# Optimization experiments

Measured on AMD Instinct MI355X. Metric: run time of the kernel, lower is better.

The kernel has to match this reference:

```python
import jax, jax.numpy as jnp
import numpy as np

H = 768
NH = 12
HD = H // NH


def setup_inputs() -> dict:
    key = jax.random.key(0)
    ks = jax.random.split(key, 12)
    B, S = 2, 2048
    s = 1.0 / np.sqrt(H)
    inp = {
        "hidden_states": jax.random.normal(ks[0], (B, S, H), dtype=jnp.float32),
        "attention_mask": jnp.ones((B, S), dtype=jnp.float32),
        "Wq": jax.random.normal(ks[1], (H, H), dtype=jnp.float32) * s,
        "bq": jnp.zeros((H,), dtype=jnp.float32),
        "Wk": jax.random.normal(ks[2], (H, H), dtype=jnp.float32) * s,
        "bk": jnp.zeros((H,), dtype=jnp.float32),
        "Wv": jax.random.normal(ks[3], (H, H), dtype=jnp.float32) * s,
        "bv": jnp.zeros((H,), dtype=jnp.float32),
        "Wo": jax.random.normal(ks[4], (H, H), dtype=jnp.float32) * s,
        "bo": jnp.zeros((H,), dtype=jnp.float32),
        "ln_gamma": jnp.ones((H,), dtype=jnp.float32),
        "ln_beta": jnp.zeros((H,), dtype=jnp.float32),
    }
    return inp


def _split_heads(x):
    # [B,S,H] -> [B,NH,S,HD]
    B, S, _ = x.shape
    return x.reshape(B, S, NH, HD).transpose(0, 2, 1, 3)


def reference(hidden_states, attention_mask, Wq, bq, Wk, bk, Wv, bv, Wo, bo, ln_gamma, ln_beta):
    x = hidden_states
    q = _split_heads(x @ Wq.T + bq)
    k = _split_heads(x @ Wk.T + bk)
    v = _split_heads(x @ Wv.T + bv)
    # scores: [B,NH,S,S]
    scores = jnp.einsum("bhqd,bhkd->bhqk", q, k) / jnp.sqrt(jnp.float32(HD))
    mask = (1.0 - attention_mask)[:, None, None, :] * -10000.0
    scores = scores + mask
    probs = jax.nn.softmax(scores, axis=-1)  # dropout is identity at inference
    ctx = jnp.einsum("bhqk,bhkd->bhqd", probs, v)
    B, _, S, _ = ctx.shape
    ctx = ctx.transpose(0, 2, 1, 3).reshape(B, S, H)
    out = ctx @ Wo.T + bo
    y = out + x
    mu = jnp.mean(y, axis=-1, keepdims=True)
    var = jnp.var(y, axis=-1, keepdims=True)
    y = (y - mu) / jnp.sqrt(var + 1e-5)
    return y * ln_gamma + ln_beta
```

## Files before the change

kernel.cpp:

```cpp
#include <hip/hip_runtime.h>
#include <math.h>

#define HH 768
#define NHEADS 12
#define HDIM 64
#define SEQ 2048
#define NB 2
#define L2E 1.44269504088896f

typedef __attribute__((ext_vector_type(8))) short s8v;
typedef __attribute__((ext_vector_type(4))) short s4v;
typedef __attribute__((ext_vector_type(4))) float f4v;

static __device__ inline short f2bf(float f) {
    union { float f; unsigned u; } v; v.f = f;
    unsigned r = v.u + 0x7fff + ((v.u >> 16) & 1);
    return (short)(r >> 16);
}

#if __has_builtin(__builtin_amdgcn_exp2f)
#define EXP2(x) __builtin_amdgcn_exp2f(x)
#else
#define EXP2(x) __expf((x) * 0.6931471805599453f)
#endif

__device__ __forceinline__ unsigned cvt_pk_bf16(float a, float b) {
    unsigned r;
    asm("v_cvt_pk_bf16_f32 %0, %1, %2" : "=v"(r) : "v"(a), "v"(b));
    return r;
}

__device__ __forceinline__ void gld16(const void* g, void* l) {
    __builtin_amdgcn_global_load_lds(
        (const __attribute__((address_space(1))) void*)g,
        (__attribute__((address_space(3))) void*)l, 16, 0, 0);
}

#define XV8   393216
#define WV8   73728
__global__ __launch_bounds__(256)
void cvt_kernel(const float* __restrict__ X, short* __restrict__ Xb,
                const float* __restrict__ W0, short* __restrict__ W0b,
                const float* __restrict__ W1, short* __restrict__ W1b,
                const float* __restrict__ W2, short* __restrict__ W2b,
                const float* __restrict__ W3, short* __restrict__ W3b)
{
    int gid = blockIdx.x * 256 + threadIdx.x;
    const float* src; short* dst; size_t off;
    if      (gid < XV8)            { src = X;  dst = Xb;  off = gid; }
    else if (gid < XV8 + WV8)      { src = W0; dst = W0b; off = gid - XV8; }
    else if (gid < XV8 + 2*WV8)    { src = W1; dst = W1b; off = gid - XV8 - WV8; }
    else if (gid < XV8 + 3*WV8)    { src = W2; dst = W2b; off = gid - XV8 - 2*WV8; }
    else if (gid < XV8 + 4*WV8)    { src = W3; dst = W3b; off = gid - XV8 - 3*WV8; }
    else return;
    off *= 8;
    float4 a = *(const float4*)(src + off);
    float4 b = *(const float4*)(src + off + 4);
    s8v o;
    o[0] = f2bf(a.x); o[1] = f2bf(a.y); o[2] = f2bf(a.z); o[3] = f2bf(a.w);
    o[4] = f2bf(b.x); o[5] = f2bf(b.y); o[6] = f2bf(b.z); o[7] = f2bf(b.w);
    *(s8v*)(dst + off) = o;
}

template<int EPI>
__global__ __launch_bounds__(256)
void gemm_mfma(const short* __restrict__ A,
               const short* __restrict__ Wq, const short* __restrict__ Wk,
               const short* __restrict__ Wv,
               const float* __restrict__ bq, const float* __restrict__ bk,
               const float* __restrict__ bv,
               short* __restrict__ Qo, short* __restrict__ Ko, short* __restrict__ Vo,
               const float* __restrict__ Xres, float* __restrict__ Fo)
{
    __shared__ __align__(16) short As[128*32];
    __shared__ __align__(16) short Bs[128*32];

    const int tid  = threadIdx.x;
    const int w    = tid >> 6;
    const int lane = tid & 63;
    const int g    = lane >> 4;
    const int r    = lane & 15;
    const int wr   = w >> 1;
    const int wc   = w & 1;
    const int m0   = blockIdx.y * 128;

    int n0;
    const short* Wb; const float* bias; short* outp; float scale;
    if (EPI == 0) {
        const int seg = blockIdx.x / 6;
        n0 = (blockIdx.x % 6) * 128;
        Wb   = seg == 0 ? Wq : seg == 1 ? Wk : Wv;
        bias = seg == 0 ? bq : seg == 1 ? bk : bv;
        outp = seg == 0 ? Qo : seg == 1 ? Ko : Vo;
        scale = seg == 0 ? (0.125f * L2E) : 1.0f;
    } else {
        n0 = blockIdx.x * 128;
        Wb = Wq; bias = bq; outp = nullptr; scale = 1.0f;
    }

    const int lrow = lane >> 2;
    const int lcol = (lane & 3) * 8;
    const short* Ag0 = A  + (size_t)(m0 + w*32 + lrow) * HH + lcol;
    const short* Bg0 = Wb + (size_t)(n0 + w*32 + lrow) * HH + lcol;
    short* Al0 = As + (w*32)      * 32;
    short* Al1 = As + (w*32 + 16) * 32;
    short* Bl0 = Bs + (w*32)      * 32;
    short* Bl1 = Bs + (w*32 + 16) * 32;

    f4v acc[4][4];
    #pragma unroll
    for (int i = 0; i < 4; i++)
        #pragma unroll
        for (int j = 0; j < 4; j++) acc[i][j] = (f4v){0.f,0.f,0.f,0.f};

    for (int kt = 0; kt < HH/32; ++kt) {
        const int k0 = kt * 32;
        gld16(Ag0 + k0,           Al0);
        gld16(Ag0 + k0 + 16*HH,   Al1);
        gld16(Bg0 + k0,           Bl0);
        gld16(Bg0 + k0 + 16*HH,   Bl1);
        __syncthreads();

        s8v af[4], bf[4];
        #pragma unroll
        for (int mi = 0; mi < 4; mi++)
            af[mi] = *(const s8v*)(As + (wr*64 + mi*16 + r)*32 + g*8);
        #pragma unroll
        for (int ni = 0; ni < 4; ni++)
            bf[ni] = *(const s8v*)(Bs + (wc*64 + ni*16 + r)*32 + g*8);
        __builtin_amdgcn_s_setprio(1);
        #pragma unroll
        for (int mi = 0; mi < 4; mi++)
            #pragma unroll
            for (int ni = 0; ni < 4; ni++)
                acc[mi][ni] = __builtin_amdgcn_mfma_f32_16x16x32_bf16(af[mi], bf[ni], acc[mi][ni], 0, 0, 0);
        __builtin_amdgcn_s_setprio(0);
        __syncthreads();
    }

    if (EPI == 0) {
        #pragma unroll
        for (int mi = 0; mi < 4; mi++) {
            #pragma unroll
            for (int j = 0; j < 4; j++) {
                const int m = m0 + wr*64 + mi*16 + 4*g + j;
                const int bb = m >> 11;
                const int s  = m & 2047;
                #pragma unroll
                for (int ni = 0; ni < 4; ni++) {
                    const int n = n0 + wc*64 + ni*16 + r;
                    const int h = n >> 6;
                    const int d = n & 63;
                    outp[((size_t)((bb*NHEADS + h)*SEQ) + s)*HDIM + d] =
                        f2bf((acc[mi][ni][j] + bias[n]) * scale);
                }
            }
        }
    } else {
        #pragma unroll
        for (int mi = 0; mi < 4; mi++) {
            #pragma unroll
            for (int j = 0; j < 4; j++) {
                const int m = m0 + wr*64 + mi*16 + 4*g + j;
                #pragma unroll
                for (int ni = 0; ni < 4; ni++) {
                    const int n = n0 + wc*64 + ni*16 + r;
                    Fo[(size_t)m*HH + n] = acc[mi][ni][j] + bias[n] + Xres[(size_t)m*HH + n];
                }
            }
        }
    }
}

__global__ __launch_bounds__(256)
void vtrans_kernel(const short* __restrict__ V, short* __restrict__ VT)
{
    const int st = blockIdx.x;
    const int h  = blockIdx.y;
    const int b  = blockIdx.z;
    __shared__ short T[64][72];
    const int t = threadIdx.x;
    const short* src = V + ((size_t)(b*NHEADS + h)*SEQ + st*64) * HDIM;

    {
        const int sl = t >> 2;
        const int dq = (t & 3) * 16;
        s8v a = *(const s8v*)(src + sl*HDIM + dq);
        s8v c = *(const s8v*)(src + sl*HDIM + dq + 8);
        #pragma unroll
        for (int i = 0; i < 8; i++) { T[dq+i][sl] = a[i]; T[dq+8+i][sl] = c[i]; }
    }
    __syncthreads();
    {
        const int d  = t >> 2;
        const int sq = (t & 3) * 16;
        s8v o0 = *(const s8v*)&T[d][sq];
        s8v o1 = *(const s8v*)&T[d][sq+8];
        short* dst = VT + ((size_t)(b*NHEADS + h)*HDIM + d)*SEQ + st*64 + sq;
        *(s8v*)(dst)     = o0;
        *(s8v*)(dst + 8) = o1;
    }
}

#define NPAIR (SEQ/64)
__global__ __launch_bounds__(512, 4)
void attn_mfma(const short* __restrict__ Q, const short* __restrict__ K,
               const short* __restrict__ VT, const float* __restrict__ mask,
               short* __restrict__ CTX)
{
    const int wgid = (blockIdx.x & 7) * 96 + (blockIdx.x >> 3);
    const int qt = wgid & 31;
    const int bh = wgid >> 5;
    const int h  = bh % NHEADS;
    const int b  = bh / NHEADS;

    const size_t hb = (size_t)(b * NHEADS + h);
    const short* Qg  = Q  + hb * SEQ * HDIM;
    const short* Kg  = K  + hb * SEQ * HDIM;
    const short* VTg = VT + hb * HDIM * SEQ;

    __shared__ __align__(16) char lds[49152];
    char* Kbase = lds;
    char* Vbase = lds + 16384;
    char* Pbase = lds + 32768;

    const int tid  = threadIdx.x;
    const int w    = tid >> 6;
    const int grp  = w >> 2;
    const int wq   = w & 3;
    const int lane = tid & 63;
    const int g    = lane >> 4;
    const int r    = lane & 15;
    const int q0   = qt * 64;

    const short* qrow = Qg + (size_t)(q0 + wq*16 + r) * HDIM;
    const s8v qf0 = *(const s8v*)(qrow + 8*g);
    const s8v qf1 = *(const s8v*)(qrow + 8*g + 32);

    f4v acc[4];
    #pragma unroll
    for (int t = 0; t < 4; t++) acc[t] = (f4v){0.f, 0.f, 0.f, 0.f};
    f4v lsum = (f4v){0.f, 0.f, 0.f, 0.f};

    const int srow = lane >> 3;
    const int scol = 8 * ((lane & 7) ^ srow);

    #define STAGE(PT, DB) do {                                                 \
        const int pk0 = (PT) * 64;                                             \
        char* kd = Kbase + (DB)*8192 + w*1024;                                 \
        gld16(Kg + (size_t)(pk0 + 8*w + srow)*HDIM + scol, kd);                \
        char* vd = Vbase + (DB)*8192 + w*1024;                                 \
        gld16(VTg + (size_t)(8*w + srow)*SEQ + pk0 + scol, vd);                \
    } while (0)

    STAGE(0, 0);
    __syncthreads();

    char* pb = Pbase + w*2048;

    for (int pt = 0; pt < NPAIR; ++pt) {
        const int db = pt & 1;
        if (pt + 1 < NPAIR) STAGE(pt + 1, db ^ 1);

        const char* Kc = Kbase + db*8192 + grp*4096;
        const char* Vc = Vbase + db*8192;
        const int k0 = pt*64 + grp*32;

        float madd[2];
        madd[0] = (mask[b*SEQ + k0 + r]      - 1.0f) * (10000.0f * L2E);
        madd[1] = (mask[b*SEQ + k0 + 16 + r] - 1.0f) * (10000.0f * L2E);

        f4v sj[2];
        __builtin_amdgcn_s_setprio(1);
        #pragma unroll
        for (int j = 0; j < 2; j++) {
            const int krow = 16*j + r;
            const char* kb = Kc + krow * 128;
            const int sw = (r & 7) << 4;
            s8v kf0 = *(const s8v*)(kb + ((16*g)      ^ sw));
            s8v kf1 = *(const s8v*)(kb + ((16*g + 64) ^ sw));
            f4v z = (f4v){0.f, 0.f, 0.f, 0.f};
            z = __builtin_amdgcn_mfma_f32_16x16x32_bf16(qf0, kf0, z, 0, 0, 0);
            z = __builtin_amdgcn_mfma_f32_16x16x32_bf16(qf1, kf1, z, 0, 0, 0);
            #pragma unroll
            for (int i = 0; i < 4; i++) z[i] += madd[j];
            sj[j] = z;
        }
        __builtin_amdgcn_s_setprio(0);

        #pragma unroll
        for (int j = 0; j < 2; j++)
            #pragma unroll
            for (int i = 0; i < 4; i++)
                sj[j][i] = EXP2(sj[j][i]);
        #pragma unroll
        for (int i = 0; i < 4; i++)
            lsum[i] += sj[0][i] + sj[1][i];

        #pragma unroll
        for (int i = 0; i < 4; i++) {
            const int prow = 4*g + i;
            char* base = pb + prow * 128;
            const int sw = (prow & 7) << 4;
            unsigned u = cvt_pk_bf16(sj[0][i], sj[1][i]);
            *(short*)(base + ((r*2)        ^ sw)) = (short)(u & 0xffff);
            *(short*)(base + ((32 + r*2)   ^ sw)) = (short)(u >> 16);
        }

        __builtin_amdgcn_s_setprio(1);
        {
            s8v pf = *(const s8v*)(pb + r*128 + ((16*g) ^ ((r & 7) << 4)));
            #pragma unroll
            for (int t4 = 0; t4 < 4; t4++) {
                const int vrow = 16*t4 + r;
                s8v vf = *(const s8v*)(Vc + vrow*128 + ((16*(4*grp + g)) ^ ((r & 7) << 4)));
                acc[t4] = __builtin_amdgcn_mfma_f32_16x16x32_bf16(pf, vf, acc[t4], 0, 0, 0);
            }
        }
        __builtin_amdgcn_s_setprio(0);

        __syncthreads();
    }

    if (grp == 1) {
        float* mb = (float*)(lds + wq*5120 + lane*80);
        *(f4v*)(mb)      = acc[0];
        *(f4v*)(mb + 4)  = acc[1];
        *(f4v*)(mb + 8)  = acc[2];
        *(f4v*)(mb + 12) = acc[3];
        *(f4v*)(mb + 16) = lsum;
    }
    __syncthreads();
    if (grp == 0) {
        const float* mb = (const float*)(lds + wq*5120 + lane*80);
        acc[0] += *(const f4v*)(mb);
        acc[1] += *(const f4v*)(mb + 4);
        acc[2] += *(const f4v*)(mb + 8);
        acc[3] += *(const f4v*)(mb + 12);
        lsum   += *(const f4v*)(mb + 16);

        #pragma unroll
        for (int m = 1; m <= 8; m <<= 1) {
            lsum[0] += __shfl_xor(lsum[0], m);
            lsum[1] += __shfl_xor(lsum[1], m);
            lsum[2] += __shfl_xor(lsum[2], m);
            lsum[3] += __shfl_xor(lsum[3], m);
        }

        #pragma unroll
        for (int i = 0; i < 4; i++) {
            const float invl = 1.0f / lsum[i];
            const size_t rowbase = ((size_t)(b*SEQ) + q0 + wq*16 + 4*g + i) * HH + h*HDIM;
            #pragma unroll
            for (int t4 = 0; t4 < 4; t4++)
                CTX[rowbase + 16*t4 + r] = f2bf(acc[t4][i] * invl);
        }
    }
    #undef STAGE
}

__global__ __launch_bounds__(256)
void ln_kernel(float* __restrict__ y, const float* __restrict__ gamma,
               const float* __restrict__ beta)
{
    const int row = blockIdx.x;
    float* p = y + (size_t)row * HH;
    const int tid = threadIdx.x;

    float v[3];
    float s = 0.f, ss = 0.f;
    #pragma unroll
    for (int i = 0; i < 3; i++) {
        float x = p[tid + i*256];
        v[i] = x;
        s += x;
        ss += x * x;
    }
    #pragma unroll
    for (int off = 32; off > 0; off >>= 1) {
        s  += __shfl_down(s,  off);
        ss += __shfl_down(ss, off);
    }
    __shared__ float sbuf[4], ssbuf[4];
    __shared__ float mu_s, rstd_s;
    const int wave = tid >> 6;
    if ((tid & 63) == 0) { sbuf[wave] = s; ssbuf[wave] = ss; }
    __syncthreads();
    if (tid == 0) {
        float S  = sbuf[0] + sbuf[1] + sbuf[2] + sbuf[3];
        float SS = ssbuf[0] + ssbuf[1] + ssbuf[2] + ssbuf[3];
        float mu = S * (1.0f / HH);
        float var = SS * (1.0f / HH) - mu * mu;
        mu_s = mu;
        rstd_s = rsqrtf(var + 1e-5f);
    }
    __syncthreads();
    const float mu = mu_s, rstd = rstd_s;
    #pragma unroll
    for (int i = 0; i < 3; i++) {
        const int c = tid + i*256;
        p[c] = (v[i] - mu) * rstd * gamma[c] + beta[c];
    }
}

extern "C" void kernel_launch(void* const* d_in, const int* in_sizes, int n_in,
                              void* d_out, int out_size, void* d_ws, size_t ws_size,
                              hipStream_t stream)
{
    const float* x     = (const float*)d_in[0];
    const float* mask  = (const float*)d_in[1];
    const float* Wq    = (const float*)d_in[2];
    const float* bq    = (const float*)d_in[3];
    const float* Wk    = (const float*)d_in[4];
    const float* bk    = (const float*)d_in[5];
    const float* Wv    = (const float*)d_in[6];
    const float* bv    = (const float*)d_in[7];
    const float* Wo    = (const float*)d_in[8];
    const float* bo    = (const float*)d_in[9];
    const float* gamma = (const float*)d_in[10];
    const float* beta  = (const float*)d_in[11];

    const size_t PER = (size_t)NB * NHEADS * SEQ * HDIM;
    const size_t WSZ = (size_t)HH * HH;
    short* wsS  = (short*)d_ws;
    short* Xb   = wsS;
    short* VTb  = wsS;
    short* Wqb  = wsS + PER;
    short* Wkb  = Wqb + WSZ;
    short* Wvb  = Wkb + WSZ;
    short* Wob  = Wvb + WSZ;
    short* Qb   = Wob + WSZ;
    short* Kb   = Qb + PER;
    short* Vb   = Kb + PER;
    short* CTXb = Vb;
    float* out  = (float*)d_out;

    cvt_kernel<<<2688, 256, 0, stream>>>(x, Xb, Wq, Wqb, Wk, Wkb, Wv, Wvb, Wo, Wob);

    gemm_mfma<0><<<dim3(18, 32), 256, 0, stream>>>(
        Xb, Wqb, Wkb, Wvb, bq, bk, bv, Qb, Kb, Vb, nullptr, nullptr);

    vtrans_kernel<<<dim3(SEQ/64, NHEADS, NB), 256, 0, stream>>>(Vb, VTb);

    attn_mfma<<<768, 512, 0, stream>>>(Qb, Kb, VTb, mask, CTXb);

    gemm_mfma<1><<<dim3(6, 32), 256, 0, stream>>>(
        CTXb, Wob, nullptr, nullptr, bo, nullptr, nullptr,
        nullptr, nullptr, nullptr, x, out);

    ln_kernel<<<NB*SEQ, 256, 0, stream>>>(out, gamma, beta);
}
```

Measured before the change: 123.8 us.

## Fuse V transpose into QKV GEMM epilogue and stage mask in LDS

The QKV projection epilogue now writes the V segment directly in transposed [d][s] layout using packed 4-element stores, which removes the separate vtrans kernel launch and its round trip through global memory. The attention kernel preloads the precomputed, bf16-quantized mask bias into shared memory once per block instead of reading and transforming global mask values every tile. Workspace buffers are remapped so CTX reuses the Xb region. The mask is now held in bf16, which loses some precision in the additive bias, and the transposed V stores are strided across SEQ.

```diff
diff --git a/kernel.cpp b/kernel.cpp
--- a/kernel.cpp
+++ b/kernel.cpp
@@ -85,9 +85,10 @@
     const int m0   = blockIdx.y * 128;
 
     int n0;
+    int seg = 0;
     const short* Wb; const float* bias; short* outp; float scale;
     if (EPI == 0) {
-        const int seg = blockIdx.x / 6;
+        seg = blockIdx.x / 6;
         n0 = (blockIdx.x % 6) * 128;
         Wb   = seg == 0 ? Wq : seg == 1 ? Wk : Wv;
         bias = seg == 0 ? bq : seg == 1 ? bk : bv;
@@ -139,11 +140,28 @@
     }
 
     if (EPI == 0) {
-        #pragma unroll
-        for (int mi = 0; mi < 4; mi++) {
-            #pragma unroll
-            for (int j = 0; j < 4; j++) {
-                const int m = m0 + wr*64 + mi*16 + 4*g + j;
+        if (seg < 2) {
+            #pragma unroll
+            for (int mi = 0; mi < 4; mi++) {
+                #pragma unroll
+                for (int j = 0; j < 4; j++) {
+                    const int m = m0 + wr*64 + mi*16 + 4*g + j;
+                    const int bb = m >> 11;
+                    const int s  = m & 2047;
+                    #pragma unroll
+                    for (int ni = 0; ni < 4; ni++) {
+                        const int n = n0 + wc*64 + ni*16 + r;
+                        const int h = n >> 6;
+                        const int d = n & 63;
+                        outp[((size_t)((bb*NHEADS + h)*SEQ) + s)*HDIM + d] =
+                            f2bf((acc[mi][ni][j] + bias[n]) * scale);
+                    }
+                }
+            }
+        } else {
+            #pragma unroll
+            for (int mi = 0; mi < 4; mi++) {
+                const int m  = m0 + wr*64 + mi*16 + 4*g;
                 const int bb = m >> 11;
                 const int s  = m & 2047;
                 #pragma unroll
@@ -151,8 +169,11 @@
                     const int n = n0 + wc*64 + ni*16 + r;
                     const int h = n >> 6;
                     const int d = n & 63;
-                    outp[((size_t)((bb*NHEADS + h)*SEQ) + s)*HDIM + d] =
-                        f2bf((acc[mi][ni][j] + bias[n]) * scale);
+                    s4v pk;
+                    #pragma unroll
+                    for (int j = 0; j < 4; j++)
+                        pk[j] = f2bf(acc[mi][ni][j] + bias[n]);
+                    *(s4v*)(outp + ((size_t)((bb*NHEADS + h)*HDIM) + d)*SEQ + s) = pk;
                 }
             }
         }
@@ -169,36 +190,6 @@
                 }
             }
         }
-    }
-}
-
-__global__ __launch_bounds__(256)
-void vtrans_kernel(const short* __restrict__ V, short* __restrict__ VT)
-{
-    const int st = blockIdx.x;
-    const int h  = blockIdx.y;
-    const int b  = blockIdx.z;
-    __shared__ short T[64][72];
-    const int t = threadIdx.x;
-    const short* src = V + ((size_t)(b*NHEADS + h)*SEQ + st*64) * HDIM;
-
-    {
-        const int sl = t >> 2;
-        const int dq = (t & 3) * 16;
-        s8v a = *(const s8v*)(src + sl*HDIM + dq);
-        s8v c = *(const s8v*)(src + sl*HDIM + dq + 8);
-        #pragma unroll
-        for (int i = 0; i < 8; i++) { T[dq+i][sl] = a[i]; T[dq+8+i][sl] = c[i]; }
-    }
-    __syncthreads();
-    {
-        const int d  = t >> 2;
-        const int sq = (t & 3) * 16;
-        s8v o0 = *(const s8v*)&T[d][sq];
-        s8v o1 = *(const s8v*)&T[d][sq+8];
-        short* dst = VT + ((size_t)(b*NHEADS + h)*HDIM + d)*SEQ + st*64 + sq;
-        *(s8v*)(dst)     = o0;
-        *(s8v*)(dst + 8) = o1;
     }
 }
 
@@ -219,10 +210,11 @@
     const short* Kg  = K  + hb * SEQ * HDIM;
     const short* VTg = VT + hb * HDIM * SEQ;
 
-    __shared__ __align__(16) char lds[49152];
+    __shared__ __align__(16) char lds[53248];
     char* Kbase = lds;
     char* Vbase = lds + 16384;
     char* Pbase = lds + 32768;
+    short* Mls  = (short*)(lds + 49152);
 
     const int tid  = threadIdx.x;
     const int w    = tid >> 6;
@@ -237,6 +229,16 @@
     const s8v qf0 = *(const s8v*)(qrow + 8*g);
     const s8v qf1 = *(const s8v*)(qrow + 8*g + 32);
 
+    {
+        float4 mv = *(const float4*)(mask + b*SEQ + tid*4);
+        s4v md;
+        md[0] = f2bf((mv.x - 1.0f) * (10000.0f * L2E));
+        md[1] = f2bf((mv.y - 1.0f) * (10000.0f * L2E));
+        md[2] = f2bf((mv.z - 1.0f) * (10000.0f * L2E));
+        md[3] = f2bf((mv.w - 1.0f) * (10000.0f * L2E));
+        *(s4v*)(Mls + tid*4) = md;
+    }
+
     f4v acc[4];
     #pragma unroll
     for (int t = 0; t < 4; t++) acc[t] = (f4v){0.f, 0.f, 0.f, 0.f};
@@ -267,8 +269,13 @@
         const int k0 = pt*64 + grp*32;
 
         float madd[2];
-        madd[0] = (mask[b*SEQ + k0 + r]      - 1.0f) * (10000.0f * L2E);
-        madd[1] = (mask[b*SEQ + k0 + 16 + r] - 1.0f) * (10000.0f * L2E);
+        {
+            union { unsigned u; float f; } c0, c1;
+            c0.u = ((unsigned)(unsigned short)Mls[k0 + r])      << 16;
+            c1.u = ((unsigned)(unsigned short)Mls[k0 + 16 + r]) << 16;
+            madd[0] = c0.f;
+            madd[1] = c1.f;
+        }
 
         f4v sj[2];
         __builtin_amdgcn_s_setprio(1);
@@ -424,23 +431,20 @@
     const size_t WSZ = (size_t)HH * HH;
     short* wsS  = (short*)d_ws;
     short* Xb   = wsS;
-    short* VTb  = wsS;
     short* Wqb  = wsS + PER;
     short* Wkb  = Wqb + WSZ;
     short* Wvb  = Wkb + WSZ;
     short* Wob  = Wvb + WSZ;
     short* Qb   = Wob + WSZ;
     short* Kb   = Qb + PER;
-    short* Vb   = Kb + PER;
-    short* CTXb = Vb;
+    short* VTb  = Kb + PER;
+    short* CTXb = Xb;
     float* out  = (float*)d_out;
 
     cvt_kernel<<<2688, 256, 0, stream>>>(x, Xb, Wq, Wqb, Wk, Wkb, Wv, Wvb, Wo, Wob);
 
     gemm_mfma<0><<<dim3(18, 32), 256, 0, stream>>>(
-        Xb, Wqb, Wkb, Wvb, bq, bk, bv, Qb, Kb, Vb, nullptr, nullptr);
-
-    vtrans_kernel<<<dim3(SEQ/64, NHEADS, NB), 256, 0, stream>>>(Vb, VTb);
+        Xb, Wqb, Wkb, Wvb, bq, bk, bv, Qb, Kb, VTb, nullptr, nullptr);
 
     attn_mfma<<<768, 512, 0, stream>>>(Qb, Kb, VTb, mask, CTXb);
 
```

New measurement: 121.3 us. -2.0%, faster.
